# Performance work log

Hardware: AMD Instinct MI355X
Metric: run time of the kernel (lower is better)

## Reference

```python
import jax, jax.numpy as jnp
import numpy as np

EPS = 1e-5
BIG = np.int32(2 ** 30)      # sentinel larger than any voxel label
L_MAX = 1024                  # fixed upper bound on number of components (jit-friendly)


def _offsets(conn):
    # 3D neighborhood offsets with at most `conn` nonzero coordinates (skimage connectivity)
    offs = []
    for dz in (-1, 0, 1):
        for dy in (-1, 0, 1):
            for dx in (-1, 0, 1):
                nz = (dz != 0) + (dy != 0) + (dx != 0)
                if 0 < nz <= conn:
                    offs.append((dz, dy, dx))
    return offs


def _ccl_26(fg):
    """Connected-component labeling, 26-connectivity (skimage.label connectivity=3).
    Iterative min-label propagation (3x3x3 min-pool) + pointer jumping.
    Returns int32 labels: 0 = background, each component gets min(flat_index)+1."""
    shape = fg.shape
    n = fg.size
    init = jnp.where(fg, jnp.arange(1, n + 1, dtype=jnp.int32).reshape(shape), 0)

    def step(labels):
        cand = jnp.where(fg, labels, BIG)
        pooled = jax.lax.reduce_window(cand, BIG, jax.lax.min, (3, 3, 3), (1, 1, 1), 'SAME')
        new = jnp.where(fg, jnp.minimum(labels, pooled), 0)
        flat = new.ravel()
        for _ in range(2):  # pointer jumping / path compression (labels are flat_index+1)
            parent = flat[jnp.maximum(flat - 1, 0)]
            flat = jnp.where(flat > 0, parent, 0)
        return flat.reshape(shape)

    def cond(c):
        old, new = c
        return jnp.any(old != new)

    def body(c):
        _, cur = c
        return cur, step(cur)

    _, final = jax.lax.while_loop(cond, body, (init, step(init)))
    return final


def _inner_boundary_18(fg):
    """skimage find_boundaries(mode='inner', connectivity=2) on 3D binary mask:
    foreground voxel with any background voxel in its 18-neighborhood
    (fg & ~erosion(fg), reflect border handling)."""
    D, H, W = fg.shape
    p = jnp.pad(fg, 1, mode='reflect')
    eroded = fg
    for dz, dy, dx in _offsets(2):
        eroded = eroded & p[1 + dz:1 + dz + D, 1 + dy:1 + dy + H, 1 + dx:1 + dx + W]
    return fg & ~eroded


def _compactness(y_pred):
    fg = y_pred > 0.5
    labels = _ccl_26(fg)                       # [D,H,W] int32
    boundary = _inner_boundary_18(fg)          # [D,H,W] bool

    # compact per-component ids (sorted unique labels, padded with BIG to stay sorted)
    uniq = jnp.unique(labels, size=L_MAX, fill_value=BIG)
    ids = jnp.searchsorted(uniq, labels).astype(jnp.int32)

    area = jax.ops.segment_sum(fg.astype(jnp.float32).ravel(), ids.ravel(), num_segments=L_MAX)
    perim = jax.ops.segment_sum(boundary.astype(jnp.float32).ravel(), ids.ravel(), num_segments=L_MAX)

    valid = (uniq > 0) & (uniq < BIG)
    # sum over z of 4*pi*area_z / (perim_3d^2 + eps) == 4*pi*total_area / (perim^2 + eps),
    # then averaged over depth D (as in the original per-label /= shape[0]).
    per_label = jnp.where(valid, 4.0 * jnp.pi * area / (perim ** 2 + EPS), 0.0)
    return jnp.sum(per_label) / y_pred.shape[0]


def setup_inputs() -> dict:
    key = jax.random.key(0)
    y_pred = jax.random.uniform(key, (64, 256, 256), dtype=jnp.float32)
    return {"y_pred": y_pred}


def reference(y_pred) -> jnp.ndarray:
    comp = _compactness(y_pred)
    return 1.0 / (comp + EPS)
```

## Files before the change

### kernel.cpp

```cpp
#include <hip/hip_runtime.h>

#define DD 64
#define HH 256
#define WW 256
#define NN (DD*HH*WW)
#define GHS 4096
#define NCOPY 16
#define PHS 131072
#define NSEG (NN/32)

#define TZ 8
#define TY 32
#define TX 32
#define TVOX (TZ*TY*TX)

#define CA 458752
#define CB 114688
#define CFACE (CA + 4*CB)

__device__ const signed char Foff[27][3] = {
  {-1,-1,-1},{-1,-1,0},{-1,-1,1},{-1,0,-1},{-1,0,0},{-1,0,1},{-1,1,-1},{-1,1,0},{-1,1,1},
  {-1,-1,-1},{-1,-1,0},{-1,-1,1},{0,-1,-1},{0,-1,0},{0,-1,1},
  {-1,1,-1},{-1,1,0},{-1,1,1},
  {-1,-1,-1},{-1,0,-1},{-1,1,-1},{0,-1,-1},{0,0,-1},
  {-1,-1,1},{-1,0,1},{-1,1,1},{0,-1,1}};
__device__ const int Fst[5] = {0, 9, 15, 18, 23};
__device__ const int Fct[5] = {9, 6, 3, 5, 4};

__device__ __forceinline__ int ufind(int* P, int x){
  int p = P[x];
  while (p != x){
    int gp = P[p];
    if (gp != p) P[x] = gp;
    x = gp;
    p = P[x];
  }
  return x;
}

__device__ __forceinline__ int ufind_ro(const int* P, int x){
  int p = P[x];
  while (p != x){ x = p; p = P[x]; }
  return x;
}

__device__ __forceinline__ void uunion(int* P, int a, int b){
  while (true){
    a = ufind(P, a);
    b = ufind(P, b);
    if (a == b) return;
    if (a < b){ int t = a; a = b; b = t; }
    int old = atomicMin(&P[a], b);
    if (old == a) return;
    a = old;
  }
}

__device__ __forceinline__ int run_start(unsigned m, int x){
  unsigned zb = (~m) & ((x == 0) ? 0u : ((1u << x) - 1u));
  return (zb == 0) ? 0 : (32 - __builtin_clz(zb));
}

__device__ __forceinline__ int refl(int v, int L){ return v < 0 ? 1 : (v >= L ? L - 2 : v); }

__global__ __launch_bounds__(1024) void k_local(const float* __restrict__ in,
                                                int* __restrict__ parent,
                                                unsigned* __restrict__ fgbits,
                                                int* __restrict__ hkey,
                                                int* __restrict__ harea,
                                                int* __restrict__ hper,
                                                unsigned long long* __restrict__ ph){
  __shared__ int sl[TVOX];
  __shared__ unsigned srow[256];
  const int t = threadIdx.x;
  const int b = blockIdx.x;
  const int z0 = (b >> 6) * TZ;
  const int y0 = ((b >> 3) & 7) * TY;
  const int x0 = (b & 7) * TX;

  if (b < (NCOPY * GHS) / 1024){ int j = b * 1024 + t; hkey[j] = -1; harea[j] = 0; hper[j] = 0; }
  { int j = b * 1024 + t; if (j < PHS) ph[j] = ~0ULL; }

  const int row = t >> 2;
  const int xb  = (t & 3) * 8;
  const int lz  = row >> 5, ly = row & 31;
  const int gi0 = ((z0 + lz) << 16) | ((y0 + ly) << 8) | (x0 + xb);

  float4 f0 = *(const float4*)(in + gi0);
  float4 f1 = *(const float4*)(in + gi0 + 4);
  int by = (f0.x > 0.5f)        | ((f0.y > 0.5f) << 1) |
           ((f0.z > 0.5f) << 2) | ((f0.w > 0.5f) << 3) |
           ((f1.x > 0.5f) << 4) | ((f1.y > 0.5f) << 5) |
           ((f1.z > 0.5f) << 6) | ((f1.w > 0.5f) << 7);
  int v1 = by | (__shfl_xor(by, 1) << 8);
  int v2 = v1 | (__shfl_xor(v1, 2) << 16);
  if ((t & 3) == 0){
    srow[row] = (unsigned)v2;
    fgbits[((z0 + lz) << 11) | ((y0 + ly) << 3) | (x0 >> 5)] = (unsigned)v2;
  }
  __syncthreads();

  const unsigned m = srow[row];
  const unsigned starts = m & ~(m << 1);
  const unsigned sm = starts & (0xFFu << xb);

  {
    unsigned w = sm;
    while (w){
      int s = __builtin_ctz(w); w &= w - 1;
      sl[(row << 5) | s] = (row << 5) | s;
    }
  }
  __syncthreads();

  const int rel[4][2] = {{-1,-1},{-1,0},{-1,1},{0,-1}};
  {
    unsigned w0 = sm;
    while (w0){
      int x = __builtin_ctz(w0); w0 &= w0 - 1;
      unsigned zs = (~m) >> x;
      int len = zs ? __builtin_ctz(zs) : (32 - x);
      int end = x + len - 1;
      unsigned long long wmask = ((1ull << (end + 2)) - 1) &
                                 ~((x == 0) ? 0ull : ((1ull << (x - 1)) - 1));
      int self = (row << 5) | x;
      #pragma unroll
      for (int r = 0; r < 4; r++){
        int zz = lz + rel[r][0], yy = ly + rel[r][1];
        if (zz < 0 || yy < 0 || yy >= TY) continue;
        int nrow = (zz << 5) | yy;
        unsigned mN = srow[nrow];
        unsigned wm = mN & (unsigned)wmask;
        while (wm){
          int bb = __builtin_ctz(wm);
          int ns = run_start(mN, bb);
          uunion(sl, self, (nrow << 5) | ns);
          unsigned t2 = (~mN) >> bb;
          int l2 = t2 ? __builtin_ctz(t2) : (32 - bb);
          unsigned long long clr = (bb + l2 >= 32) ? 0xffffffffull : ((1ull << (bb + l2)) - 1);
          wm &= ~(unsigned)clr;
        }
      }
    }
  }
  __syncthreads();

  {
    unsigned w = sm;
    while (w){
      int s = __builtin_ctz(w); w &= w - 1;
      int v = (row << 5) | s;
      sl[v] = ufind_ro(sl, v);
    }
  }
  __syncthreads();

  int lab[8];
  int cur = -1;
  #pragma unroll
  for (int k = 0; k < 8; k++){
    int x = xb + k;
    if (!((m >> x) & 1)){ lab[k] = -1; cur = -1; continue; }
    if (cur < 0){
      int rs = (k == 0) ? run_start(m, x) : x;
      int r = sl[(row << 5) | rs];
      cur = ((z0 + (r >> 10)) << 16) | ((y0 + ((r >> 5) & 31)) << 8) | (x0 + (r & 31));
    }
    lab[k] = cur;
  }
  *(int4*)(parent + gi0)     = make_int4(lab[0], lab[1], lab[2], lab[3]);
  *(int4*)(parent + gi0 + 4) = make_int4(lab[4], lab[5], lab[6], lab[7]);
}

__device__ __forceinline__ void phash_union(unsigned long long* H, unsigned long long key,
                                            int* parent){
  unsigned h = (unsigned)((key * 0x9E3779B97F4A7C15ull) >> 47);
  while (true){
    unsigned long long old = atomicCAS(&H[h], ~0ULL, key);
    if (old == ~0ULL){ uunion(parent, (int)(key >> 32), (int)(key & 0xffffffffu)); return; }
    if (old == key) return;
    h = (h + 1) & (PHS - 1);
  }
}

__global__ __launch_bounds__(256) void k_pairs(int* __restrict__ parent,
                                               const unsigned* __restrict__ fgbits,
                                               unsigned long long* __restrict__ ph){
  __shared__ unsigned long long pk[256];
  const int t = threadIdx.x;
  pk[t] = ~0ULL;
  __syncthreads();

  const int id = blockIdx.x * 256 + t;
  int z, y, x, ot;
  if (id < CA){ ot = 0; z = ((id >> 16) + 1) << 3; y = (id >> 8) & 255; x = id & 255; }
  else {
    int q = id - CA;
    int f = q >> 14;
    int r = q & 16383;
    int g = f / 7, mm = f % 7;
    if      (g == 0){ ot = 1; y = (mm + 1) << 5;  z = r >> 8; x = r & 255; }
    else if (g == 1){ ot = 2; y = (mm << 5) + 31; z = r >> 8; x = r & 255; }
    else if (g == 2){ ot = 3; x = (mm + 1) << 5;  z = r >> 8; y = r & 255; }
    else            { ot = 4; x = (mm << 5) + 31; z = r >> 8; y = r & 255; }
  }
  const int i = (z << 16) | (y << 8) | x;
  if ((fgbits[(z << 11) | (y << 3) | (x >> 5)] >> (x & 31)) & 1){
    int a = parent[i];
    const int st = Fst[ot], en = st + Fct[ot];
    for (int k = st; k < en; k++){
      int zz = z + Foff[k][0], yy = y + Foff[k][1], xx = x + Foff[k][2];
      if (zz < 0 || yy < 0 || yy >= HH || xx < 0 || xx >= WW) continue;
      if (!((fgbits[(zz << 11) | (yy << 3) | (xx >> 5)] >> (xx & 31)) & 1)) continue;
      int bl = parent[(zz << 16) | (yy << 8) | xx];
      int hi = a > bl ? a : bl, lo = a > bl ? bl : a;
      unsigned long long key = ((unsigned long long)(unsigned)hi << 32) | (unsigned)lo;
      unsigned h = (unsigned)((key * 0x9E3779B97F4A7C15ull) >> 56);
      bool done = false;
      for (int probe = 0; probe < 256; probe++){
        unsigned long long old = atomicCAS(&pk[h], ~0ULL, key);
        if (old == ~0ULL || old == key){ done = true; break; }
        h = (h + 1) & 255;
      }
      if (!done) phash_union(ph, key, parent);
    }
  }
  __syncthreads();
  if (pk[t] != ~0ULL) phash_union(ph, pk[t], parent);
}

__device__ __forceinline__ void ghash_add(int* hkey, int* harea, int* hper,
                                          int key, int a, int p){
  unsigned h = ((unsigned)key * 2654435761u) >> 20;
  while (true){
    int old = atomicCAS(&hkey[h], -1, key);
    if (old == -1 || old == key){
      atomicAdd(&harea[h], a);
      if (p) atomicAdd(&hper[h], p);
      return;
    }
    h = (h + 1) & (GHS - 1);
  }
}

__global__ __launch_bounds__(1024) void k_stats(const int* __restrict__ parent,
                                                const unsigned* __restrict__ fgbits,
                                                int* __restrict__ hkey,
                                                int* __restrict__ harea,
                                                int* __restrict__ hper){
  __shared__ unsigned sfg[144];
  __shared__ unsigned sbnd[32];
  __shared__ int sk[256], sa[256], sp[256];
  const int t = threadIdx.x;
  const int b = blockIdx.x;
  const int z = b >> 6;
  const int y0 = (b & 63) * 4;

  if (t < 256){ sk[t] = -1; sa[t] = 0; sp[t] = 0; }
  if (t < 144){
    int p = t / 48, q = (t / 8) % 6, s = t & 7;
    int zz = refl(z + p - 1, DD), yy = refl(y0 + q - 1, HH);
    sfg[t] = fgbits[(zz << 11) | (yy << 3) | s];
  }
  __syncthreads();

  if (t < 32){
    int ry = t >> 3, s = t & 7;
    auto W  = [&](int p, int q){ return sfg[p * 48 + q * 8 + s]; };
    auto WL = [&](int p, int q){
      unsigned w = W(p, q);
      unsigned c = (s > 0) ? ((sfg[p * 48 + q * 8 + s - 1] >> 31) & 1u) : ((w >> 1) & 1u);
      return (w << 1) | c;
    };
    auto WR = [&](int p, int q){
      unsigned w = W(p, q);
      unsigned c = (s < 7) ? ((sfg[p * 48 + q * 8 + s + 1] & 1u) << 31) : ((w & 0x40000000u) << 1);
      return (w >> 1) | c;
    };
    int qm = ry, qc = ry + 1, qp = ry + 2;
    unsigned own = W(1, qc);
    unsigned e = W(0, qm) & W(0, qp) & W(2, qm) & W(2, qp);
    e &= W(0, qc) & WL(0, qc) & WR(0, qc);
    e &= W(2, qc) & WL(2, qc) & WR(2, qc);
    e &= W(1, qm) & WL(1, qm) & WR(1, qm);
    e &= W(1, qp) & WL(1, qp) & WR(1, qp);
    e &= WL(1, qc) & WR(1, qc);
    sbnd[t] = own & ~e;
  }
  __syncthreads();

  const int i = b * 1024 + t;
  int lab = parent[i];
  int bnd = 0;
  if (lab >= 0){
    bnd = (sbnd[t >> 5] >> (t & 31)) & 1;
    int p = parent[lab];
    while (p != lab){ lab = p; p = parent[lab]; }
  }

  const int lane = t & 63;
  unsigned long long fgm = __ballot(lab >= 0);
  unsigned long long bm  = __ballot(bnd != 0);
  unsigned long long act = fgm;
  while (act){
    int leader = (int)__ffsll(act) - 1;
    int llab = __shfl(lab, leader);
    unsigned long long match = __ballot(lab == llab) & fgm;
    if (lane == leader){
      int a = (int)__popcll(match);
      int p = (int)__popcll(match & bm);
      unsigned h = ((unsigned)llab * 2654435761u) >> 24;
      bool done = false;
      for (int probe = 0; probe < 256; probe++){
        int old = atomicCAS(&sk[h], -1, llab);
        if (old == -1 || old == llab){
          atomicAdd(&sa[h], a);
          if (p) atomicAdd(&sp[h], p);
          done = true; break;
        }
        h = (h + 1) & 255;
      }
      if (!done) ghash_add(hkey, harea, hper, llab, a, p);
    }
    act &= ~match;
  }
  __syncthreads();
  const int c = (b & (NCOPY - 1)) * GHS;
  if (t < 256 && sk[t] >= 0) ghash_add(hkey + c, harea + c, hper + c, sk[t], sa[t], sp[t]);
}

__global__ __launch_bounds__(256) void k_merge(int* __restrict__ hkey,
                                               int* __restrict__ harea,
                                               int* __restrict__ hper){
  const int j = GHS + blockIdx.x * 256 + threadIdx.x;
  int key = hkey[j];
  if (key >= 0) ghash_add(hkey, harea, hper, key, harea[j], hper[j]);
}

__global__ __launch_bounds__(256) void k_fin(const int* __restrict__ hkey,
                                             const int* __restrict__ harea,
                                             const int* __restrict__ hper,
                                             float* __restrict__ out){
  __shared__ float ssum[256];
  const int t = threadIdx.x;
  float s = 0.0f;
  for (int j = t; j < GHS; j += 256){
    if (hkey[j] >= 0){
      float a = (float)harea[j];
      float p = (float)hper[j];
      s += 12.566370614359172f * a / (p * p + 1e-5f);
    }
  }
  ssum[t] = s;
  __syncthreads();
  for (int w = 128; w > 0; w >>= 1){
    if (t < w) ssum[t] += ssum[t + w];
    __syncthreads();
  }
  if (t == 0){
    float comp = ssum[0] / 64.0f;
    out[0] = 1.0f / (comp + 1e-5f);
  }
}

extern "C" void kernel_launch(void* const* d_in, const int* in_sizes, int n_in,
                              void* d_out, int out_size, void* d_ws, size_t ws_size,
                              hipStream_t stream){
  const float* y = (const float*)d_in[0];
  char* w = (char*)d_ws;
  int* parent            = (int*)w;                    w += (size_t)NN * 4;
  unsigned long long* ph = (unsigned long long*)w;     w += (size_t)PHS * 8;
  int* hkey              = (int*)w;                    w += (size_t)NCOPY * GHS * 4;
  int* harea             = (int*)w;                    w += (size_t)NCOPY * GHS * 4;
  int* hper              = (int*)w;                    w += (size_t)NCOPY * GHS * 4;
  unsigned* fgbits       = (unsigned*)w;               w += (size_t)NSEG * 4;
  float* out = (float*)d_out;

  hipLaunchKernelGGL(k_local, dim3(512),       dim3(1024), 0, stream, y, parent, fgbits, hkey, harea, hper, ph);
  hipLaunchKernelGGL(k_pairs, dim3(CFACE/256), dim3(256),  0, stream, parent, fgbits, ph);
  hipLaunchKernelGGL(k_stats, dim3(NN/1024),   dim3(1024), 0, stream, parent, fgbits, hkey, harea, hper);
  hipLaunchKernelGGL(k_merge, dim3((NCOPY-1)*GHS/256), dim3(256), 0, stream, hkey, harea, hper);
  hipLaunchKernelGGL(k_fin,   dim3(1),         dim3(256),  0, stream, hkey, harea, hper, out);
}
```

Baseline: 161.0 us.

## Store union-find parents per run instead of per voxel

```diff
diff --git a/kernel.cpp b/kernel.cpp
--- a/kernel.cpp
+++ b/kernel.cpp
@@ -8,11 +8,11 @@
 #define NCOPY 16
 #define PHS 131072
 #define NSEG (NN/32)
+#define NRUN (NSEG*16)
 
 #define TZ 8
 #define TY 32
 #define TX 32
-#define TVOX (TZ*TY*TX)
 
 #define CA 458752
 #define CB 114688
@@ -35,12 +35,6 @@
     x = gp;
     p = P[x];
   }
-  return x;
-}
-
-__device__ __forceinline__ int ufind_ro(const int* P, int x){
-  int p = P[x];
-  while (p != x){ x = p; p = P[x]; }
   return x;
 }
 
@@ -56,21 +50,56 @@
   }
 }
 
+__device__ __forceinline__ int slp(int v){ return ((v >> 5) * 33) + (v & 31); }
+
+__device__ __forceinline__ int lfind_ro(const int* P, int x){
+  int p = P[slp(x)];
+  while (p != x){ x = p; p = P[slp(x)]; }
+  return x;
+}
+
+__device__ __forceinline__ int lfind(int* P, int x){
+  int p = P[slp(x)];
+  while (p != x){
+    int gp = P[slp(p)];
+    if (gp != p) P[slp(x)] = gp;
+    x = gp;
+    p = P[slp(x)];
+  }
+  return x;
+}
+
+__device__ __forceinline__ void lunion(int* P, int a, int b){
+  while (true){
+    a = lfind(P, a);
+    b = lfind(P, b);
+    if (a == b) return;
+    if (a < b){ int t = a; a = b; b = t; }
+    int old = atomicMin(&P[slp(a)], b);
+    if (old == a) return;
+    a = old;
+  }
+}
+
 __device__ __forceinline__ int run_start(unsigned m, int x){
   unsigned zb = (~m) & ((x == 0) ? 0u : ((1u << x) - 1u));
   return (zb == 0) ? 0 : (32 - __builtin_clz(zb));
 }
 
+__device__ __forceinline__ int run_idx(unsigned starts, int x){
+  return __popc(starts & ((2u << x) - 1u)) - 1;
+}
+
 __device__ __forceinline__ int refl(int v, int L){ return v < 0 ? 1 : (v >= L ? L - 2 : v); }
 
 __global__ __launch_bounds__(1024) void k_local(const float* __restrict__ in,
-                                                int* __restrict__ parent,
+                                                int* __restrict__ runp,
                                                 unsigned* __restrict__ fgbits,
                                                 int* __restrict__ hkey,
                                                 int* __restrict__ harea,
                                                 int* __restrict__ hper,
                                                 unsigned long long* __restrict__ ph){
-  __shared__ int sl[TVOX];
+  __shared__ int sl[33 * 256];
   __shared__ unsigned srow[256];
   const int t = threadIdx.x;
   const int b = blockIdx.x;
@@ -108,7 +137,7 @@
     unsigned w = sm;
     while (w){
       int s = __builtin_ctz(w); w &= w - 1;
-      sl[(row << 5) | s] = (row << 5) | s;
+      sl[slp((row << 5) | s)] = (row << 5) | s;
     }
   }
   __syncthreads();
@@ -134,7 +163,7 @@
         while (wm){
           int bb = __builtin_ctz(wm);
           int ns = run_start(mN, bb);
-          uunion(sl, self, (nrow << 5) | ns);
+          lunion(sl, self, (nrow << 5) | ns);
           unsigned t2 = (~mN) >> bb;
           int l2 = t2 ? __builtin_ctz(t2) : (32 - bb);
           unsigned long long clr = (bb + l2 >= 32) ? 0xffffffffull : ((1ull << (bb + l2)) - 1);
@@ -145,45 +174,34 @@
   }
   __syncthreads();
 
+  const int gseg = ((z0 + lz) << 11) | ((y0 + ly) << 3) | (x0 >> 5);
   {
     unsigned w = sm;
     while (w){
       int s = __builtin_ctz(w); w &= w - 1;
       int v = (row << 5) | s;
-      sl[v] = ufind_ro(sl, v);
-    }
-  }
-  __syncthreads();
-
-  int lab[8];
-  int cur = -1;
-  #pragma unroll
-  for (int k = 0; k < 8; k++){
-    int x = xb + k;
-    if (!((m >> x) & 1)){ lab[k] = -1; cur = -1; continue; }
-    if (cur < 0){
-      int rs = (k == 0) ? run_start(m, x) : x;
-      int r = sl[(row << 5) | rs];
-      cur = ((z0 + (r >> 10)) << 16) | ((y0 + ((r >> 5) & 31)) << 8) | (x0 + (r & 31));
-    }
-    lab[k] = cur;
-  }
-  *(int4*)(parent + gi0)     = make_int4(lab[0], lab[1], lab[2], lab[3]);
-  *(int4*)(parent + gi0 + 4) = make_int4(lab[4], lab[5], lab[6], lab[7]);
+      int r = lfind_ro(sl, v);
+      int rrow = r >> 5, rx = r & 31;
+      unsigned mr = srow[rrow];
+      unsigned str = mr & ~(mr << 1);
+      int rseg = ((z0 + (rrow >> 5)) << 11) | ((y0 + (rrow & 31)) << 3) | (x0 >> 5);
+      runp[(gseg << 4) + run_idx(starts, s)] = (rseg << 4) + run_idx(str, rx);
+    }
+  }
 }
 
 __device__ __forceinline__ void phash_union(unsigned long long* H, unsigned long long key,
-                                            int* parent){
+                                            int* runp){
   unsigned h = (unsigned)((key * 0x9E3779B97F4A7C15ull) >> 47);
   while (true){
     unsigned long long old = atomicCAS(&H[h], ~0ULL, key);
-    if (old == ~0ULL){ uunion(parent, (int)(key >> 32), (int)(key & 0xffffffffu)); return; }
+    if (old == ~0ULL){ uunion(runp, (int)(key >> 32), (int)(key & 0xffffffffu)); return; }
     if (old == key) return;
     h = (h + 1) & (PHS - 1);
   }
 }
 
-__global__ __launch_bounds__(256) void k_pairs(int* __restrict__ parent,
+__global__ __launch_bounds__(256) void k_pairs(int* __restrict__ runp,
                                                const unsigned* __restrict__ fgbits,
                                                unsigned long long* __restrict__ ph){
   __shared__ unsigned long long pk[256];
@@ -204,17 +222,25 @@
     else if (g == 2){ ot = 3; x = (mm + 1) << 5;  z = r >> 8; y = r & 255; }
     else            { ot = 4; x = (mm << 5) + 31; z = r >> 8; y = r & 255; }
   }
-  const int i = (z << 16) | (y << 8) | x;
-  if ((fgbits[(z << 11) | (y << 3) | (x >> 5)] >> (x & 31)) & 1){
-    int a = parent[i];
+  const int segS = (z << 11) | (y << 3) | (x >> 5);
+  const unsigned mS = fgbits[segS];
+  if ((mS >> (x & 31)) & 1){
+    const unsigned stS = mS & ~(mS << 1);
+    const int a = runp[(segS << 4) + run_idx(stS, x & 31)];
+    unsigned long long lastkey = ~0ULL;
     const int st = Fst[ot], en = st + Fct[ot];
     for (int k = st; k < en; k++){
       int zz = z + Foff[k][0], yy = y + Foff[k][1], xx = x + Foff[k][2];
       if (zz < 0 || yy < 0 || yy >= HH || xx < 0 || xx >= WW) continue;
-      if (!((fgbits[(zz << 11) | (yy << 3) | (xx >> 5)] >> (xx & 31)) & 1)) continue;
-      int bl = parent[(zz << 16) | (yy << 8) | xx];
+      int segN = (zz << 11) | (yy << 3) | (xx >> 5);
+      unsigned mN = fgbits[segN];
+      if (!((mN >> (xx & 31)) & 1)) continue;
+      unsigned stN = mN & ~(mN << 1);
+      int bl = runp[(segN << 4) + run_idx(stN, xx & 31)];
       int hi = a > bl ? a : bl, lo = a > bl ? bl : a;
       unsigned long long key = ((unsigned long long)(unsigned)hi << 32) | (unsigned)lo;
+      if (key == lastkey) continue;
+      lastkey = key;
       unsigned h = (unsigned)((key * 0x9E3779B97F4A7C15ull) >> 56);
       bool done = false;
       for (int probe = 0; probe < 256; probe++){
@@ -222,11 +248,11 @@
         if (old == ~0ULL || old == key){ done = true; break; }
         h = (h + 1) & 255;
       }
-      if (!done) phash_union(ph, key, parent);
-    }
-  }
-  __syncthreads();
-  if (pk[t] != ~0ULL) phash_union(ph, pk[t], parent);
+      if (!done) phash_union(ph, key, runp);
+    }
+  }
+  __syncthreads();
+  if (pk[t] != ~0ULL) phash_union(ph, pk[t], runp);
 }
 
 __device__ __forceinline__ void ghash_add(int* hkey, int* harea, int* hper,
@@ -243,7 +269,7 @@
   }
 }
 
-__global__ __launch_bounds__(1024) void k_stats(const int* __restrict__ parent,
+__global__ __launch_bounds__(1024) void k_stats(const int* __restrict__ runp,
                                                 const unsigned* __restrict__ fgbits,
                                                 int* __restrict__ hkey,
                                                 int* __restrict__ harea,
@@ -289,13 +315,17 @@
   }
   __syncthreads();
 
-  const int i = b * 1024 + t;
-  int lab = parent[i];
-  int bnd = 0;
-  if (lab >= 0){
+  const int x = t & 255, ry = t >> 8;
+  const unsigned m = sfg[48 + (ry + 1) * 8 + (x >> 5)];
+  int lab = -1, bnd = 0;
+  if ((m >> (x & 31)) & 1){
     bnd = (sbnd[t >> 5] >> (t & 31)) & 1;
-    int p = parent[lab];
-    while (p != lab){ lab = p; p = parent[lab]; }
+    unsigned st = m & ~(m << 1);
+    int gseg = (z << 11) | ((y0 + ry) << 3) | (x >> 5);
+    int idr = (gseg << 4) + run_idx(st, x & 31);
+    lab = runp[idr];
+    int p = runp[lab];
+    while (p != lab){ lab = p; p = runp[lab]; }
   }
 
   const int lane = t & 63;
@@ -368,7 +398,7 @@
                               hipStream_t stream){
   const float* y = (const float*)d_in[0];
   char* w = (char*)d_ws;
-  int* parent            = (int*)w;                    w += (size_t)NN * 4;
+  int* runp              = (int*)w;                    w += (size_t)NRUN * 4;
   unsigned long long* ph = (unsigned long long*)w;     w += (size_t)PHS * 8;
   int* hkey              = (int*)w;                    w += (size_t)NCOPY * GHS * 4;
   int* harea             = (int*)w;                    w += (size_t)NCOPY * GHS * 4;
@@ -376,9 +406,9 @@
   unsigned* fgbits       = (unsigned*)w;               w += (size_t)NSEG * 4;
   float* out = (float*)d_out;
 
-  hipLaunchKernelGGL(k_local, dim3(512),       dim3(1024), 0, stream, y, parent, fgbits, hkey, harea, hper, ph);
-  hipLaunchKernelGGL(k_pairs, dim3(CFACE/256), dim3(256),  0, stream, parent, fgbits, ph);
-  hipLaunchKernelGGL(k_stats, dim3(NN/1024),   dim3(1024), 0, stream, parent, fgbits, hkey, harea, hper);
+  hipLaunchKernelGGL(k_local, dim3(512),       dim3(1024), 0, stream, y, runp, fgbits, hkey, harea, hper, ph);
+  hipLaunchKernelGGL(k_pairs, dim3(CFACE/256), dim3(256),  0, stream, runp, fgbits, ph);
+  hipLaunchKernelGGL(k_stats, dim3(NN/1024),   dim3(1024), 0, stream, runp, fgbits, hkey, harea, hper);
   hipLaunchKernelGGL(k_merge, dim3((NCOPY-1)*GHS/256), dim3(256), 0, stream, hkey, harea, hper);
   hipLaunchKernelGGL(k_fin,   dim3(1),         dim3(256),  0, stream, hkey, harea, hper, out);
 }
```

Measured after the change: 170.0 us. 1.06x slower.

## Balance local union-find via shared run queue and prune face neighbor checks

Applied to the files above, without the earlier changes.

```diff
diff --git a/kernel.cpp b/kernel.cpp
--- a/kernel.cpp
+++ b/kernel.cpp
@@ -17,15 +17,6 @@
 #define CA 458752
 #define CB 114688
 #define CFACE (CA + 4*CB)
-
-__device__ const signed char Foff[27][3] = {
-  {-1,-1,-1},{-1,-1,0},{-1,-1,1},{-1,0,-1},{-1,0,0},{-1,0,1},{-1,1,-1},{-1,1,0},{-1,1,1},
-  {-1,-1,-1},{-1,-1,0},{-1,-1,1},{0,-1,-1},{0,-1,0},{0,-1,1},
-  {-1,1,-1},{-1,1,0},{-1,1,1},
-  {-1,-1,-1},{-1,0,-1},{-1,1,-1},{0,-1,-1},{0,0,-1},
-  {-1,-1,1},{-1,0,1},{-1,1,1},{0,-1,1}};
-__device__ const int Fst[5] = {0, 9, 15, 18, 23};
-__device__ const int Fct[5] = {9, 6, 3, 5, 4};
 
 __device__ __forceinline__ int ufind(int* P, int x){
   int p = P[x];
@@ -72,7 +63,10 @@
                                                 unsigned long long* __restrict__ ph){
   __shared__ int sl[TVOX];
   __shared__ unsigned srow[256];
+  __shared__ int q[4096];
+  __shared__ int qn;
   const int t = threadIdx.x;
+  const int lane = t & 63;
   const int b = blockIdx.x;
   const int z0 = (b >> 6) * TZ;
   const int y0 = ((b >> 3) & 7) * TY;
@@ -80,6 +74,7 @@
 
   if (b < (NCOPY * GHS) / 1024){ int j = b * 1024 + t; hkey[j] = -1; harea[j] = 0; hper[j] = 0; }
   { int j = b * 1024 + t; if (j < PHS) ph[j] = ~0ULL; }
+  if (t == 0) qn = 0;
 
   const int row = t >> 2;
   const int xb  = (t & 3) * 8;
@@ -105,53 +100,63 @@
   const unsigned sm = starts & (0xFFu << xb);
 
   {
-    unsigned w = sm;
-    while (w){
-      int s = __builtin_ctz(w); w &= w - 1;
-      sl[(row << 5) | s] = (row << 5) | s;
-    }
-  }
-  __syncthreads();
-
-  const int rel[4][2] = {{-1,-1},{-1,0},{-1,1},{0,-1}};
-  {
-    unsigned w0 = sm;
-    while (w0){
-      int x = __builtin_ctz(w0); w0 &= w0 - 1;
-      unsigned zs = (~m) >> x;
-      int len = zs ? __builtin_ctz(zs) : (32 - x);
-      int end = x + len - 1;
-      unsigned long long wmask = ((1ull << (end + 2)) - 1) &
-                                 ~((x == 0) ? 0ull : ((1ull << (x - 1)) - 1));
-      int self = (row << 5) | x;
-      #pragma unroll
-      for (int r = 0; r < 4; r++){
-        int zz = lz + rel[r][0], yy = ly + rel[r][1];
-        if (zz < 0 || yy < 0 || yy >= TY) continue;
-        int nrow = (zz << 5) | yy;
-        unsigned mN = srow[nrow];
-        unsigned wm = mN & (unsigned)wmask;
-        while (wm){
-          int bb = __builtin_ctz(wm);
-          int ns = run_start(mN, bb);
-          uunion(sl, self, (nrow << 5) | ns);
-          unsigned t2 = (~mN) >> bb;
-          int l2 = t2 ? __builtin_ctz(t2) : (32 - bb);
-          unsigned long long clr = (bb + l2 >= 32) ? 0xffffffffull : ((1ull << (bb + l2)) - 1);
-          wm &= ~(unsigned)clr;
-        }
-      }
-    }
-  }
-  __syncthreads();
-
-  {
+    int cnt = __popc(sm);
+    int pre = cnt;
+    #pragma unroll
+    for (int d = 1; d < 64; d <<= 1){
+      int v = __shfl_up(pre, d);
+      if (lane >= d) pre += v;
+    }
+    int tot = __shfl(pre, 63);
+    int bw = 0;
+    if (lane == 63) bw = atomicAdd(&qn, tot);
+    bw = __shfl(bw, 63);
+    int pos = bw + pre - cnt;
     unsigned w = sm;
     while (w){
       int s = __builtin_ctz(w); w &= w - 1;
       int v = (row << 5) | s;
-      sl[v] = ufind_ro(sl, v);
-    }
+      sl[v] = v;
+      q[pos++] = v;
+    }
+  }
+  __syncthreads();
+  const int NQ = qn;
+
+  const int rel[4][2] = {{-1,-1},{-1,0},{-1,1},{0,-1}};
+  for (int it = t; it < NQ; it += 1024){
+    int v = q[it];
+    int vrow = v >> 5, x = v & 31;
+    unsigned mr = srow[vrow];
+    unsigned zs = (~mr) >> x;
+    int len = zs ? __builtin_ctz(zs) : (32 - x);
+    int end = x + len - 1;
+    unsigned long long wmask = ((1ull << (end + 2)) - 1) &
+                               ~((x == 0) ? 0ull : ((1ull << (x - 1)) - 1));
+    int vlz = vrow >> 5, vly = vrow & 31;
+    #pragma unroll
+    for (int r = 0; r < 4; r++){
+      int zz = vlz + rel[r][0], yy = vly + rel[r][1];
+      if (zz < 0 || yy < 0 || yy >= TY) continue;
+      int nrow = (zz << 5) | yy;
+      unsigned mN = srow[nrow];
+      unsigned wm = mN & (unsigned)wmask;
+      while (wm){
+        int bb = __builtin_ctz(wm);
+        int ns = run_start(mN, bb);
+        uunion(sl, v, (nrow << 5) | ns);
+        unsigned t2 = (~mN) >> bb;
+        int l2 = t2 ? __builtin_ctz(t2) : (32 - bb);
+        unsigned long long clr = (bb + l2 >= 32) ? 0xffffffffull : ((1ull << (bb + l2)) - 1);
+        wm &= ~(unsigned)clr;
+      }
+    }
+  }
+  __syncthreads();
+
+  for (int it = t; it < NQ; it += 1024){
+    int v = q[it];
+    sl[v] = ufind_ro(sl, v);
   }
   __syncthreads();
 
@@ -204,25 +209,53 @@
     else if (g == 2){ ot = 3; x = (mm + 1) << 5;  z = r >> 8; y = r & 255; }
     else            { ot = 4; x = (mm << 5) + 31; z = r >> 8; y = r & 255; }
   }
-  const int i = (z << 16) | (y << 8) | x;
-  if ((fgbits[(z << 11) | (y << 3) | (x >> 5)] >> (x & 31)) & 1){
-    int a = parent[i];
-    const int st = Fst[ot], en = st + Fct[ot];
-    for (int k = st; k < en; k++){
-      int zz = z + Foff[k][0], yy = y + Foff[k][1], xx = x + Foff[k][2];
-      if (zz < 0 || yy < 0 || yy >= HH || xx < 0 || xx >= WW) continue;
-      if (!((fgbits[(zz << 11) | (yy << 3) | (xx >> 5)] >> (xx & 31)) & 1)) continue;
-      int bl = parent[(zz << 16) | (yy << 8) | xx];
+  const int s = x >> 5, xl = x & 31;
+  const unsigned wself = fgbits[(z << 11) | (y << 3) | s];
+  if ((wself >> xl) & 1){
+    const int a = parent[(z << 16) | (y << 8) | x];
+    unsigned long long lastkey = ~0ULL;
+
+    auto do_pair = [&](int zz, int yy, int xc){
+      int bl = parent[(zz << 16) | (yy << 8) | xc];
       int hi = a > bl ? a : bl, lo = a > bl ? bl : a;
       unsigned long long key = ((unsigned long long)(unsigned)hi << 32) | (unsigned)lo;
+      if (key == lastkey) return;
+      lastkey = key;
       unsigned h = (unsigned)((key * 0x9E3779B97F4A7C15ull) >> 56);
-      bool done = false;
       for (int probe = 0; probe < 256; probe++){
         unsigned long long old = atomicCAS(&pk[h], ~0ULL, key);
-        if (old == ~0ULL || old == key){ done = true; break; }
+        if (old == ~0ULL || old == key) return;
         h = (h + 1) & 255;
       }
-      if (!done) phash_union(ph, key, parent);
+      phash_union(ph, key, parent);
+    };
+
+    auto do_row = [&](int zz, int yy){
+      if (zz < 0 || yy < 0 || yy >= HH) return;
+      unsigned mN = fgbits[(zz << 11) | (yy << 3) | s];
+      if ((mN >> xl) & 1){ do_pair(zz, yy, x); return; }
+      bool l = (xl > 0) ? ((mN >> (xl - 1)) & 1)
+                        : (x > 0 && ((fgbits[(zz << 11) | (yy << 3) | (s - 1)] >> 31) & 1));
+      bool r = (xl < 31) ? ((mN >> (xl + 1)) & 1)
+                         : (x < WW - 1 && (fgbits[(zz << 11) | (yy << 3) | (s + 1)] & 1));
+      if (l) do_pair(zz, yy, x - 1);
+      if (r) do_pair(zz, yy, x + 1);
+    };
+
+    auto do_bit = [&](int zz, int yy, int xc){
+      if (zz < 0 || yy < 0 || yy >= HH) return;
+      unsigned mN = fgbits[(zz << 11) | (yy << 3) | (xc >> 5)];
+      if ((mN >> (xc & 31)) & 1) do_pair(zz, yy, xc);
+    };
+
+    switch (ot){
+      case 0: do_row(z-1, y-1); do_row(z-1, y); do_row(z-1, y+1); break;
+      case 1: do_row(z-1, y-1); do_row(z, y-1); break;
+      case 2: do_row(z-1, y+1); break;
+      case 3: do_bit(z-1, y-1, x-1); do_bit(z-1, y, x-1); do_bit(z-1, y+1, x-1);
+              do_bit(z,   y-1, x-1); do_bit(z,   y, x-1); break;
+      case 4: do_bit(z-1, y-1, x+1); do_bit(z-1, y, x+1); do_bit(z-1, y+1, x+1);
+              do_bit(z,   y-1, x+1); break;
     }
   }
   __syncthreads();
```

Measured after the change: 152.4 us (median of 2 runs). -5.4%, faster.
